# Kernel optimization log

Measured on AMD Instinct MI355X. Metric: run time of the kernel, lower is better.

## Reference

```python
import jax, jax.numpy as jnp
import numpy as np

# ---- config (mirrors argparse-config of dnc_model) ----
T, B, IN = 64, 32, 64          # time-major input [T,B,IN]
N, Wd, R, NW = 512, 64, 4, 1   # memory_size, word_size, num_reads, num_writes
H, OUT = 256, 64               # controller hidden, output_size
CLIP = 20.0
EPS = 1e-6
IF = R*Wd + R + NW*Wd + NW + NW*Wd + NW*Wd + R + NW + NW + R*(1+2*NW)  # interface size = 471
CTRL_IN = IN + R*Wd


def setup_inputs() -> dict:
    key = jax.random.key(0)
    ks = jax.random.split(key, 6)
    g = lambda k, shape, s: (jax.random.normal(k, shape, jnp.float32) * s)
    return {
        "inputs": g(ks[0], (T, B, IN), 1.0),
        "Wx": g(ks[1], (CTRL_IN, 4*H), 0.05),
        "Wh": g(ks[2], (H, 4*H), 0.05),
        "b_lstm": jnp.zeros((4*H,), jnp.float32),
        "W_if": g(ks[3], (H, IF), 0.05),
        "b_if": jnp.zeros((IF,), jnp.float32),
        "W_out": g(ks[4], (H + R*Wd, OUT), 0.05),
        "b_out": jnp.zeros((OUT,), jnp.float32),
    }


def _clip(x):
    return jnp.clip(x, -CLIP, CLIP)


def _oneplus(x):
    return 1.0 + jax.nn.softplus(x)


def _content_weights(memory, keys, strengths):
    # memory [B,N,Wd], keys [B,K,Wd], strengths [B,K] -> softmax cosine weights [B,K,N]
    dot = jnp.einsum('bkw,bnw->bkn', keys, memory)
    mn = jnp.sqrt(jnp.sum(memory * memory, -1))          # [B,N]
    kn = jnp.sqrt(jnp.sum(keys * keys, -1))              # [B,K]
    sim = dot / (kn[..., None] * mn[:, None, :] + EPS)
    return jax.nn.softmax(sim * strengths[..., None], axis=-1)


def _allocation(usage):
    # usage [B,N] -> allocation weights [B,N] (sorted-free-list scheme)
    u = EPS + (1.0 - EPS) * usage
    idx = jnp.argsort(u, axis=-1)                        # ascending usage
    su = jnp.take_along_axis(u, idx, -1)
    cp = jnp.cumprod(su, axis=-1)
    excl = jnp.concatenate([jnp.ones_like(cp[:, :1]), cp[:, :-1]], -1)
    a_sorted = (1.0 - su) * excl
    inv = jnp.argsort(idx, axis=-1)
    return jnp.take_along_axis(a_sorted, inv, -1)


def _dnc_forward(inputs, Wx, Wh, b_lstm, W_if, b_if, W_out, b_out):
    eye = jnp.eye(N, dtype=inputs.dtype)

    def step(carry, x_t):
        h, c, mem, rw, ww_prev, link, prec, usage, reads = carry
        # ---- controller LSTM (prev read vectors fed in) ----
        ctrl_in = jnp.concatenate([x_t, reads.reshape(B, R*Wd)], -1)
        gates = ctrl_in @ Wx + h @ Wh + b_lstm
        ig, fg, gg, og = jnp.split(gates, 4, -1)
        c = jax.nn.sigmoid(fg) * c + jax.nn.sigmoid(ig) * jnp.tanh(gg)
        h = jax.nn.sigmoid(og) * jnp.tanh(c)
        hc, cc = _clip(h), _clip(c)
        # ---- interface vector ----
        itf = hc @ W_if + b_if
        off = 0
        read_keys = itf[:, off:off+R*Wd].reshape(B, R, Wd); off += R*Wd
        read_str = _oneplus(itf[:, off:off+R]); off += R
        write_keys = itf[:, off:off+NW*Wd].reshape(B, NW, Wd); off += NW*Wd
        write_str = _oneplus(itf[:, off:off+NW]); off += NW
        erase = jax.nn.sigmoid(itf[:, off:off+NW*Wd]).reshape(B, NW, Wd); off += NW*Wd
        write_vecs = itf[:, off:off+NW*Wd].reshape(B, NW, Wd); off += NW*Wd
        free_g = jax.nn.sigmoid(itf[:, off:off+R]); off += R
        alloc_g = jax.nn.sigmoid(itf[:, off:off+NW]); off += NW
        write_g = jax.nn.sigmoid(itf[:, off:off+NW]); off += NW
        modes = jax.nn.softmax(itf[:, off:off+R*(1+2*NW)].reshape(B, R, 1+2*NW), -1)
        bwd_mode = modes[..., :NW]
        fwd_mode = modes[..., NW:2*NW]
        content_mode = modes[..., 2*NW]
        # ---- usage update (uses prev write/read weights) ----
        u = usage + (1.0 - usage) * (1.0 - jnp.prod(1.0 - ww_prev, axis=1))
        psi = jnp.prod(1.0 - free_g[..., None] * rw, axis=1)
        usage = u * psi
        # ---- write weights: allocation + content ----
        allocs = []
        u_run = usage
        for hd in range(NW):
            a = _allocation(u_run)
            allocs.append(a)
            u_run = u_run + (1.0 - u_run) * (write_g[:, hd:hd+1] * alloc_g[:, hd:hd+1]) * a
        alloc = jnp.stack(allocs, 1)                      # [B,NW,N]
        wc = _content_weights(mem, write_keys, write_str) # [B,NW,N]
        ww = write_g[..., None] * (alloc_g[..., None] * alloc + (1.0 - alloc_g[..., None]) * wc)
        # ---- erase / add write ----
        erase_w = ww[..., None] * erase[:, :, None, :]    # [B,NW,N,Wd]
        mem = mem * jnp.prod(1.0 - erase_w, axis=1) + jnp.einsum('bhn,bhw->bnw', ww, write_vecs)
        # ---- temporal link + precedence ----
        w_i = ww[..., :, None]
        w_j = ww[..., None, :]
        link = (1.0 - w_i - w_j) * link + w_i * prec[..., None, :]
        link = link * (1.0 - eye)
        prec = (1.0 - ww.sum(-1, keepdims=True)) * prec + ww
        # ---- read weights: content + forward/backward linkage ----
        rc = _content_weights(mem, read_keys, read_str)   # [B,R,N]
        fw = jnp.einsum('bhij,brj->brhi', link, rw)       # forward  [B,R,NW,N]
        bw = jnp.einsum('bhji,brj->brhi', link, rw)       # backward [B,R,NW,N]
        rw = (content_mode[..., None] * rc
              + jnp.einsum('brh,brhn->brn', fwd_mode, fw)
              + jnp.einsum('brh,brhn->brn', bwd_mode, bw))
        reads = jnp.einsum('brn,bnw->brw', rw, mem)       # [B,R,Wd]
        out = _clip(jnp.concatenate([hc, reads.reshape(B, R*Wd)], -1) @ W_out + b_out)
        return (hc, cc, mem, rw, ww, link, prec, usage, reads), out

    z = jnp.zeros
    dt = inputs.dtype
    carry0 = (z((B, H), dt), z((B, H), dt), z((B, N, Wd), dt), z((B, R, N), dt),
              z((B, NW, N), dt), z((B, NW, N, N), dt), z((B, NW, N), dt),
              z((B, N), dt), z((B, R, Wd), dt))
    _, outs = jax.lax.scan(step, carry0, inputs)
    return outs  # [T, B, OUT]


def reference(inputs, Wx, Wh, b_lstm, W_if, b_if, W_out, b_out):
    return _dnc_forward(inputs, Wx, Wh, b_lstm, W_if, b_if, W_out, b_out)
```

## Files before the change

kernel.cpp:

```cpp
#include <hip/hip_runtime.h>
#include <math.h>

#define Tn 64
#define Bn 32
#define INn 64
#define Nn 512
#define WDn 64
#define Rn 4
#define Hn 256
#define G4H 1024
#define OUTn 64
#define IFn 471
#define CLIPV 20.0f
#define EPSV 1e-6f

#define OFF_RKEY 0
#define OFF_RSTR 256
#define OFF_WKEY 260
#define OFF_WSTR 324
#define OFF_ERASE 325
#define OFF_WVEC 389
#define OFF_FREE 453
#define OFF_AG 457
#define OFF_WG 458
#define OFF_MODES 459

__device__ float S_h[2][Bn][Hn];
__device__ float S_c[2][Bn][Hn];
__device__ float S_gates[2][Bn][G4H];
__device__ float S_mem[Bn][Nn][WDn];
__device__ float S_rw[Bn][Rn][Nn];
__device__ float S_ww[2][Bn][Nn];
__device__ float S_link[Bn][Nn][Nn];
__device__ float S_prec[2][Bn][Nn];
__device__ float S_usage[2][Bn][Nn];
__device__ float S_reads[Bn][Rn][WDn];
__device__ float S_itf[Bn][IFn];
__device__ float S_rc[Bn][Rn][Nn];
__device__ float S_fw[Bn][Rn][Nn];
__device__ float S_bwp[Bn][8][Rn*Nn];
__device__ float S_sumww[Bn];
__device__ unsigned int g_ww[Bn];
__device__ unsigned int g_rc[Bn];
__device__ unsigned int g_ld[Bn];
__device__ unsigned int g_fin;

__device__ __forceinline__ float sigm(float x){ return 1.f/(1.f+expf(-x)); }
__device__ __forceinline__ float clipv(float x){ return fminf(fmaxf(x,-CLIPV),CLIPV); }
__device__ __forceinline__ float oneplusf(float x){
  float sp = (x > 0.f) ? (x + log1pf(expf(-x))) : log1pf(expf(x));
  return 1.f + sp;
}
__device__ __forceinline__ float wredsum(float v){
  #pragma unroll
  for (int o=32;o>0;o>>=1) v += __shfl_xor(v,o,64);
  return v;
}
__device__ __forceinline__ float bredsum(float v, volatile float* scr){
  v = wredsum(v);
  if ((threadIdx.x & 63) == 0) scr[threadIdx.x >> 6] = v;
  __syncthreads();
  float s = scr[0];
  #pragma unroll
  for (int i=1;i<8;i++) s += scr[i];
  __syncthreads();
  return s;
}
__device__ __forceinline__ float bredmax(float v, volatile float* scr){
  #pragma unroll
  for (int o=32;o>0;o>>=1) v = fmaxf(v,__shfl_xor(v,o,64));
  if ((threadIdx.x & 63) == 0) scr[threadIdx.x >> 6] = v;
  __syncthreads();
  float m = scr[0];
  #pragma unroll
  for (int i=1;i<8;i++) m = fmaxf(m, scr[i]);
  __syncthreads();
  return m;
}
__device__ __forceinline__ void sig_release(unsigned int* flag){
  __builtin_amdgcn_fence(__ATOMIC_RELEASE, "agent");
  __hip_atomic_fetch_add(flag, 1u, __ATOMIC_RELAXED, __HIP_MEMORY_SCOPE_AGENT);
}
__device__ __forceinline__ void spin_until(unsigned int* flag, unsigned int target){
  while (__hip_atomic_load(flag, __ATOMIC_RELAXED, __HIP_MEMORY_SCOPE_AGENT) < target)
    __builtin_amdgcn_s_sleep(8);
}

extern "C" __global__ void __launch_bounds__(256)
k_init(){
  size_t g = (size_t)blockIdx.x*256 + threadIdx.x;
  size_t stride = (size_t)gridDim.x*256;
  float* lk = &S_link[0][0][0];
  for (size_t i=g; i<(size_t)Bn*Nn*Nn; i+=stride) lk[i]=0.f;
  float* mm = &S_mem[0][0][0];
  for (size_t i=g; i<(size_t)Bn*Nn*WDn; i+=stride) mm[i]=0.f;
  float* rr = &S_rw[0][0][0];
  for (size_t i=g; i<(size_t)Bn*Rn*Nn; i+=stride) rr[i]=0.f;
  float* rd = &S_reads[0][0][0];
  for (size_t i=g; i<(size_t)Bn*Rn*WDn; i+=stride) rd[i]=0.f;
  for (size_t i=g; i<(size_t)2*Bn*Nn; i+=stride){
    S_ww[0][0][i]=0.f; S_prec[0][0][i]=0.f; S_usage[0][0][i]=0.f;
  }
  for (size_t i=g; i<(size_t)2*Bn*Hn; i+=stride){
    S_h[0][0][i]=0.f; S_c[0][0][i]=0.f;
  }
  if (blockIdx.x==0){
    if (threadIdx.x < Bn){ g_ww[threadIdx.x]=0u; g_rc[threadIdx.x]=0u; g_ld[threadIdx.x]=0u; }
    if (threadIdx.x == 0) g_fin=0u;
  }
}

struct ShG { float ctrl[Bn][65]; };

__device__ __forceinline__ void gates_core(ShG& sg, int tn, int jt,
        const float* __restrict__ xin, const float* __restrict__ Wx,
        const float* __restrict__ Wh, const float* __restrict__ b_lstm){
  const int tid = threadIdx.x, lane = tid & 63, wvi = tid >> 6;
  const int j = jt*64 + lane;
  const int hp = (tn+1)&1;
  const int b0 = wvi*4;
  float bias = b_lstm[j];
  float a0=bias, a1=bias, a2=bias, a3=bias;
  for (int c=0;c<9;++c){
    #pragma unroll
    for (int u=0;u<4;u++){
      int e = u*512 + tid;
      int b2 = e >> 6, kk = e & 63;
      float v;
      if (c==0)       v = xin[((size_t)tn*Bn + b2)*INn + kk];
      else if (c<5)   v = ((const float*)S_reads[b2])[(c-1)*64 + kk];
      else            v = S_h[hp][b2][(c-5)*64 + kk];
      sg.ctrl[b2][kk] = v;
    }
    __syncthreads();
    const float* wb = (c<5) ? (Wx + (size_t)(c*64)*G4H + j)
                            : (Wh + (size_t)((c-5)*64)*G4H + j);
    #pragma unroll
    for (int kk=0;kk<64;kk++){
      float wv = wb[(size_t)kk*G4H];
      a0 += sg.ctrl[b0+0][kk]*wv;
      a1 += sg.ctrl[b0+1][kk]*wv;
      a2 += sg.ctrl[b0+2][kk]*wv;
      a3 += sg.ctrl[b0+3][kk]*wv;
    }
    __syncthreads();
  }
  const int gs = tn&1;
  S_gates[gs][b0+0][j]=a0;
  S_gates[gs][b0+1][j]=a1;
  S_gates[gs][b0+2][j]=a2;
  S_gates[gs][b0+3][j]=a3;
}

extern "C" __global__ void __launch_bounds__(512)
k_gates_pro(const float* __restrict__ xin, const float* __restrict__ Wx,
            const float* __restrict__ Wh, const float* __restrict__ b_lstm){
  __shared__ ShG sg;
  gates_core(sg, 0, blockIdx.x, xin, Wx, Wh, b_lstm);
}

struct ShA {
  float hc[Hn];
  float itf[IFn];
  unsigned long long keys[Nn];
  float alloc[Nn];
  float sim[Nn];
  float rsim[Rn][Nn];
  float tile[64][65];
  float wkey[WDn];
  float rk[Rn][WDn];
  float er[WDn];
  float wv[WDn];
  float red[8];
  float knw, knr[Rn], betar[Rn];
};
struct ShL {
  float ww[Nn];
  float prec[Nn];
  float rw[Rn][Nn];
  float bwp4[4][Rn][Nn];
};
struct ShF {
  float fw[Rn][Nn];
  float bw[Rn][Nn];
  float rc[Rn][Nn];
  float modes[Rn][4];
  float part[8][Rn][WDn];
  float vin[512];
};
union ShU { ShA a; ShL l; ShF f; ShG g; };

extern "C" __global__ void __launch_bounds__(512, 4)
k_step(int t, const float* __restrict__ xin,
       const float* __restrict__ Wx, const float* __restrict__ Wh,
       const float* __restrict__ b_lstm,
       const float* __restrict__ W_if, const float* __restrict__ b_if,
       const float* __restrict__ W_out, const float* __restrict__ b_out,
       float* __restrict__ outp){
  __shared__ ShU sh;
  const int tid = threadIdx.x;
  const int lane = tid & 63, wvi = tid >> 6;
  const int bid = blockIdx.x;
  const int cur = t&1, prev = cur^1;

  if (bid < 32){
    const int b = bid;
    if (tid < Hn){
      int h = tid;
      float g0=S_gates[cur][b][h],     g1=S_gates[cur][b][Hn+h];
      float g2=S_gates[cur][b][2*Hn+h],g3=S_gates[cur][b][3*Hn+h];
      float cold = S_c[prev][b][h];
      float cn = sigm(g1)*cold + sigm(g0)*tanhf(g2);
      float hn = sigm(g3)*tanhf(cn);
      float hcv = clipv(hn);
      S_c[cur][b][h] = clipv(cn);
      S_h[cur][b][h] = hcv;
      sh.a.hc[h] = hcv;
    }
    __syncthreads();
    if (tid < IFn){
      float acc = b_if[tid];
      for (int k=0;k<Hn;k+=8){
        float s = 0.f;
        #pragma unroll
        for (int u=0;u<8;u++) s += sh.a.hc[k+u]*W_if[(size_t)(k+u)*IFn + tid];
        acc += s;
      }
      sh.a.itf[tid] = acc;
      S_itf[b][tid] = acc;
    }
    __syncthreads();
    if (tid < WDn){
      sh.a.wkey[tid] = sh.a.itf[OFF_WKEY+tid];
      sh.a.er[tid]   = sigm(sh.a.itf[OFF_ERASE+tid]);
      sh.a.wv[tid]   = sh.a.itf[OFF_WVEC+tid];
    } else if (tid < WDn + Rn*WDn){
      int k2 = tid - WDn;
      sh.a.rk[k2>>6][k2&63] = sh.a.itf[OFF_RKEY + k2];
    }
    {
      float fg0=sigm(sh.a.itf[OFF_FREE+0]), fg1=sigm(sh.a.itf[OFF_FREE+1]);
      float fg2=sigm(sh.a.itf[OFF_FREE+2]), fg3=sigm(sh.a.itf[OFF_FREE+3]);
      int n = tid;
      float uu = S_usage[prev][b][n], wwp = S_ww[prev][b][n];
      float u = uu + (1.f-uu)*wwp;
      float psi = (1.f - fg0*S_rw[b][0][n])*(1.f - fg1*S_rw[b][1][n])
                * (1.f - fg2*S_rw[b][2][n])*(1.f - fg3*S_rw[b][3][n]);
      float un = u*psi;
      S_usage[cur][b][n] = un;
      float v = EPSV + (1.f-EPSV)*un;
      sh.a.keys[n] = ((unsigned long long)__float_as_uint(v) << 32) | (unsigned)n;
    }
    __syncthreads();
    if (wvi==0){
      float kv = sh.a.wkey[lane];
      float s2 = wredsum(kv*kv);
      if (lane==0) sh.a.knw = sqrtf(s2);
    } else if (wvi<=4){
      int r = wvi-1;
      float kv = sh.a.rk[r][lane];
      float s2 = wredsum(kv*kv);
      if (lane==0) sh.a.knr[r] = sqrtf(s2);
    } else if (wvi==5 && lane<4){
      sh.a.betar[lane] = oneplusf(sh.a.itf[OFF_RSTR+lane]);
    }
    {
      unsigned long long myk = sh.a.keys[tid];
      float prod = 1.f;
      for (int j=0;j<Nn;j+=8){
        #pragma unroll
        for (int u=0;u<8;u++){
          unsigned long long kj = sh.a.keys[j+u];
          float uj = __uint_as_float((unsigned)(kj>>32));
          prod *= (kj < myk) ? uj : 1.f;
        }
      }
      float myu = __uint_as_float((unsigned)(myk>>32));
      sh.a.alloc[tid] = (1.f - myu)*prod;
    }
    __syncthreads();
    float betaw = oneplusf(sh.a.itf[OFF_WSTR]);
    for (int tile=0;tile<8;tile++){
      #pragma unroll
      for (int u=0;u<8;u++){
        int e = u*512 + tid;
        int nn = e>>6, w = e&63;
        sh.a.tile[nn][w] = S_mem[b][tile*64+nn][w];
      }
      __syncthreads();
      {
        int nn = tid>>3, qq = tid&7;
        float d=0.f, nrm=0.f;
        #pragma unroll
        for (int i=0;i<8;i++){
          int w = qq*8+i;
          float m = sh.a.tile[nn][w];
          d += m*sh.a.wkey[w]; nrm += m*m;
        }
        #pragma unroll
        for (int o=1;o<8;o<<=1){ d += __shfl_xor(d,o,64); nrm += __shfl_xor(nrm,o,64); }
        if (qq==0){
          int n = tile*64+nn;
          sh.a.sim[n] = betaw * d / (sh.a.knw*sqrtf(nrm) + EPSV);
        }
      }
      __syncthreads();
    }
    {
      float v = sh.a.sim[tid];
      float mx = bredmax(v, sh.a.red);
      float e = expf(v - mx);
      float ssum = bredsum(e, sh.a.red);
      float wc = e/ssum;
      float ag = sigm(sh.a.itf[OFF_AG]);
      float wg = sigm(sh.a.itf[OFF_WG]);
      float wwv = wg*(ag*sh.a.alloc[tid] + (1.f-ag)*wc);
      S_ww[cur][b][tid] = wwv;
      float wsum = bredsum(wwv, sh.a.red);
      if (tid==0) S_sumww[b] = wsum;
      sh.a.alloc[tid] = wwv;
    }
    __syncthreads();
    if (tid==0) sig_release(&g_ww[b]);
    for (int tile=0;tile<8;tile++){
      #pragma unroll
      for (int u=0;u<8;u++){
        int e = u*512 + tid;
        int nn = e>>6, w = e&63;
        int n = tile*64+nn;
        float m = S_mem[b][n][w];
        float wwn = sh.a.alloc[n];
        m = m*(1.f - wwn*sh.a.er[w]) + wwn*sh.a.wv[w];
        S_mem[b][n][w] = m;
        sh.a.tile[nn][w] = m;
      }
      __syncthreads();
      {
        int nn = tid>>3, qq = tid&7;
        float a0=0.f,a1=0.f,a2=0.f,a3=0.f,nrm=0.f;
        #pragma unroll
        for (int i=0;i<8;i++){
          int w = qq*8+i;
          float m = sh.a.tile[nn][w];
          a0 += m*sh.a.rk[0][w]; a1 += m*sh.a.rk[1][w];
          a2 += m*sh.a.rk[2][w]; a3 += m*sh.a.rk[3][w];
          nrm += m*m;
        }
        #pragma unroll
        for (int o=1;o<8;o<<=1){
          a0 += __shfl_xor(a0,o,64); a1 += __shfl_xor(a1,o,64);
          a2 += __shfl_xor(a2,o,64); a3 += __shfl_xor(a3,o,64);
          nrm += __shfl_xor(nrm,o,64);
        }
        if (qq==0){
          int n = tile*64+nn;
          float mn = sqrtf(nrm);
          sh.a.rsim[0][n] = sh.a.betar[0]*a0/(sh.a.knr[0]*mn + EPSV);
          sh.a.rsim[1][n] = sh.a.betar[1]*a1/(sh.a.knr[1]*mn + EPSV);
          sh.a.rsim[2][n] = sh.a.betar[2]*a2/(sh.a.knr[2]*mn + EPSV);
          sh.a.rsim[3][n] = sh.a.betar[3]*a3/(sh.a.knr[3]*mn + EPSV);
        }
      }
      __syncthreads();
    }
    for (int r=0;r<Rn;r++){
      float v = sh.a.rsim[r][tid];
      float mx = bredmax(v, sh.a.red);
      float e = expf(v - mx);
      float ssum = bredsum(e, sh.a.red);
      S_rc[b][r][tid] = e/ssum;
    }
    __syncthreads();
    if (tid==0) sig_release(&g_rc[b]);

  } else if (bid < 288){
    const int idx = bid - 32;
    const int b = idx >> 3, ch = idx & 7;
    const int i0 = ch*64;
    if (tid==0){
      spin_until(&g_ww[b], (unsigned)(t+1));
      __builtin_amdgcn_fence(__ATOMIC_ACQUIRE, "agent");
    }
    __syncthreads();
    sh.l.ww[tid]   = S_ww[cur][b][tid];
    sh.l.prec[tid] = S_prec[prev][b][tid];
    for (int k=tid;k<Rn*Nn;k+=512) ((float*)sh.l.rw)[k] = ((const float*)S_rw[b])[k];
    __syncthreads();
    float sumww = S_sumww[b];
    float wj[2][4], pj[2][4], rj[4][2][4];
    #pragma unroll
    for (int jjc=0;jjc<2;jjc++){
      float4 w4 = ((const float4*)sh.l.ww)[jjc*64+lane];
      float4 p4 = ((const float4*)sh.l.prec)[jjc*64+lane];
      wj[jjc][0]=w4.x; wj[jjc][1]=w4.y; wj[jjc][2]=w4.z; wj[jjc][3]=w4.w;
      pj[jjc][0]=p4.x; pj[jjc][1]=p4.y; pj[jjc][2]=p4.z; pj[jjc][3]=p4.w;
      #pragma unroll
      for (int r=0;r<4;r++){
        float4 r4 = ((const float4*)sh.l.rw[r])[jjc*64+lane];
        rj[r][jjc][0]=r4.x; rj[r][jjc][1]=r4.y; rj[r][jjc][2]=r4.z; rj[r][jjc][3]=r4.w;
      }
    }
    float bwa[4][2][4];
    #pragma unroll
    for (int r=0;r<4;r++)
      #pragma unroll
      for (int jjc=0;jjc<2;jjc++)
        #pragma unroll
        for (int s=0;s<4;s++) bwa[r][jjc][s]=0.f;
    for (int rr=0;rr<8;rr++){
      const int i = i0 + wvi*8 + rr;
      float wi = sh.l.ww[i];
      float ci = 1.f - wi;
      float ri[4] = {sh.l.rw[0][i], sh.l.rw[1][i], sh.l.rw[2][i], sh.l.rw[3][i]};
      float f[4] = {0.f,0.f,0.f,0.f};
      float4* lrow4 = (float4*)(&S_link[b][i][0]);
      #pragma unroll
      for (int jjc=0;jjc<2;jjc++){
        float4 L4 = lrow4[jjc*64+lane];
        float Ls[4] = {L4.x, L4.y, L4.z, L4.w};
        #pragma unroll
        for (int s=0;s<4;s++){
          float Ln = (ci - wj[jjc][s])*Ls[s] + wi*pj[jjc][s];
          int j = jjc*256 + lane*4 + s;
          Ln = (j==i) ? 0.f : Ln;
          Ls[s] = Ln;
          #pragma unroll
          for (int r=0;r<4;r++){
            f[r] += Ln*rj[r][jjc][s];
            bwa[r][jjc][s] += Ln*ri[r];
          }
        }
        float4 Lo; Lo.x=Ls[0]; Lo.y=Ls[1]; Lo.z=Ls[2]; Lo.w=Ls[3];
        lrow4[jjc*64+lane] = Lo;
      }
      #pragma unroll
      for (int r=0;r<4;r++){
        float fr = wredsum(f[r]);
        if (lane==0) S_fw[b][r][i] = fr;
      }
    }
    if (wvi < 4){
      #pragma unroll
      for (int r=0;r<4;r++)
        #pragma unroll
        for (int jjc=0;jjc<2;jjc++){
          float4 v4; v4.x=bwa[r][jjc][0]; v4.y=bwa[r][jjc][1]; v4.z=bwa[r][jjc][2]; v4.w=bwa[r][jjc][3];
          ((float4*)sh.l.bwp4[wvi][r])[jjc*64+lane] = v4;
        }
    }
    __syncthreads();
    if (wvi >= 4){
      int v = wvi-4;
      #pragma unroll
      for (int r=0;r<4;r++)
        #pragma unroll
        for (int jjc=0;jjc<2;jjc++){
          float4 v4 = ((float4*)sh.l.bwp4[v][r])[jjc*64+lane];
          v4.x+=bwa[r][jjc][0]; v4.y+=bwa[r][jjc][1]; v4.z+=bwa[r][jjc][2]; v4.w+=bwa[r][jjc][3];
          ((float4*)sh.l.bwp4[v][r])[jjc*64+lane] = v4;
        }
    }
    __syncthreads();
    for (int k=tid;k<Rn*Nn;k+=512){
      float s = ((float*)sh.l.bwp4[0])[k] + ((float*)sh.l.bwp4[1])[k]
              + ((float*)sh.l.bwp4[2])[k] + ((float*)sh.l.bwp4[3])[k];
      S_bwp[b][ch][k] = s;
    }
    if (tid < 64){
      int j = i0 + tid;
      S_prec[cur][b][j] = (1.f - sumww)*sh.l.prec[j] + sh.l.ww[j];
    }
    __syncthreads();
    if (tid==0) sig_release(&g_ld[b]);

  } else if (bid < 320){
    const int b = bid - 288;
    if (tid==0){
      spin_until(&g_ld[b], 8u*(unsigned)(t+1));
      spin_until(&g_rc[b], (unsigned)(t+1));
      __builtin_amdgcn_fence(__ATOMIC_ACQUIRE, "agent");
    }
    __syncthreads();
    for (int k=tid;k<Rn*Nn;k+=512){
      ((float*)sh.f.fw)[k] = ((const float*)S_fw[b])[k];
      float sbw = 0.f;
      #pragma unroll
      for (int ch=0;ch<8;ch++) sbw += S_bwp[b][ch][k];
      ((float*)sh.f.bw)[k] = sbw;
      ((float*)sh.f.rc)[k] = ((const float*)S_rc[b])[k];
    }
    if (tid < 4){
      int r = tid;
      float m0 = S_itf[b][OFF_MODES + r*3 + 0];
      float m1 = S_itf[b][OFF_MODES + r*3 + 1];
      float m2 = S_itf[b][OFF_MODES + r*3 + 2];
      float mx = fmaxf(m0,fmaxf(m1,m2));
      float e0=expf(m0-mx), e1=expf(m1-mx), e2=expf(m2-mx);
      float si = e0+e1+e2;
      sh.f.modes[r][0]=e0/si; sh.f.modes[r][1]=e1/si; sh.f.modes[r][2]=e2/si;
    }
    __syncthreads();
    for (int k=tid;k<Rn*Nn;k+=512){
      int r = k>>9, n = k&511;
      float v = sh.f.modes[r][2]*sh.f.rc[r][n] + sh.f.modes[r][1]*sh.f.fw[r][n]
              + sh.f.modes[r][0]*sh.f.bw[r][n];
      sh.f.rc[r][n] = v;
      S_rw[b][r][n] = v;
    }
    __syncthreads();
    {
      float a0=0.f,a1=0.f,a2=0.f,a3=0.f;
      #pragma unroll 4
      for (int nn=0;nn<64;nn++){
        int n = wvi*64+nn;
        float m = S_mem[b][n][lane];
        a0 += sh.f.rc[0][n]*m; a1 += sh.f.rc[1][n]*m;
        a2 += sh.f.rc[2][n]*m; a3 += sh.f.rc[3][n]*m;
      }
      sh.f.part[wvi][0][lane]=a0; sh.f.part[wvi][1][lane]=a1;
      sh.f.part[wvi][2][lane]=a2; sh.f.part[wvi][3][lane]=a3;
    }
    __syncthreads();
    if (tid < 256){
      int r = tid>>6, w = tid&63;
      float sv = 0.f;
      #pragma unroll
      for (int v=0;v<8;v++) sv += sh.f.part[v][r][w];
      S_reads[b][r][w] = sv;
      sh.f.vin[256+tid] = sv;
      sh.f.vin[tid] = S_h[cur][b][tid];
    }
    __syncthreads();
    {
      int qq = tid>>6, o = tid&63;
      float sacc = 0.f;
      for (int k2=qq*64;k2<qq*64+64;k2+=8){
        #pragma unroll
        for (int u=0;u<8;u++) sacc += sh.f.vin[k2+u]*W_out[(size_t)(k2+u)*OUTn + o];
      }
      sh.f.part[qq][0][o] = sacc;
    }
    __syncthreads();
    if (tid < 64){
      float sv = b_out[tid];
      #pragma unroll
      for (int qq=0;qq<8;qq++) sv += sh.f.part[qq][0][tid];
      outp[((size_t)t*Bn + b)*OUTn + tid] = clipv(sv);
    }
    __syncthreads();
    if (tid==0) sig_release(&g_fin);

  } else {
    if (t+1 >= Tn) return;
    const int jt = bid - 320;
    if (tid==0){
      spin_until(&g_fin, 32u*(unsigned)(t+1));
      __builtin_amdgcn_fence(__ATOMIC_ACQUIRE, "agent");
    }
    __syncthreads();
    gates_core(sh.g, t+1, jt, xin, Wx, Wh, b_lstm);
  }
}

extern "C" void kernel_launch(void* const* d_in, const int* in_sizes, int n_in,
                              void* d_out, int out_size, void* d_ws, size_t ws_size,
                              hipStream_t stream){
  (void)in_sizes; (void)n_in; (void)d_ws; (void)ws_size; (void)out_size;
  const float* xin = (const float*)d_in[0];
  const float* Wx  = (const float*)d_in[1];
  const float* Wh  = (const float*)d_in[2];
  const float* bl  = (const float*)d_in[3];
  const float* Wif = (const float*)d_in[4];
  const float* bif = (const float*)d_in[5];
  const float* Wo  = (const float*)d_in[6];
  const float* bo  = (const float*)d_in[7];
  hipLaunchKernelGGL(k_init, dim3(1024), dim3(256), 0, stream);
  hipLaunchKernelGGL(k_gates_pro, dim3(16), dim3(512), 0, stream, xin, Wx, Wh, bl);
  for (int t=0; t<Tn; ++t){
    hipLaunchKernelGGL(k_step, dim3(336), dim3(512), 0, stream,
                       t, xin, Wx, Wh, bl, Wif, bif, Wo, bo, (float*)d_out);
  }
}
```

Measured before the change: 7.154 ms.

## Fuse per-timestep launches into one persistent kernel with flag-based dependencies

```diff
diff --git a/kernel.cpp b/kernel.cpp
--- a/kernel.cpp
+++ b/kernel.cpp
@@ -40,10 +40,13 @@
 __device__ float S_fw[Bn][Rn][Nn];
 __device__ float S_bwp[Bn][8][Rn*Nn];
 __device__ float S_sumww[Bn];
+__device__ unsigned int g_hh;
 __device__ unsigned int g_ww[Bn];
 __device__ unsigned int g_rc[Bn];
 __device__ unsigned int g_ld[Bn];
+__device__ unsigned int g_fb[Bn];
 __device__ unsigned int g_fin;
+__device__ unsigned int g_gate;
 
 __device__ __forceinline__ float sigm(float x){ return 1.f/(1.f+expf(-x)); }
 __device__ __forceinline__ float clipv(float x){ return fminf(fmaxf(x,-CLIPV),CLIPV); }
@@ -83,7 +86,23 @@
 }
 __device__ __forceinline__ void spin_until(unsigned int* flag, unsigned int target){
   while (__hip_atomic_load(flag, __ATOMIC_RELAXED, __HIP_MEMORY_SCOPE_AGENT) < target)
-    __builtin_amdgcn_s_sleep(8);
+    __builtin_amdgcn_s_sleep(2);
+}
+__device__ __forceinline__ void wait_acq1(unsigned int* f, unsigned int tgt){
+  if (threadIdx.x==0){
+    spin_until(f, tgt);
+    __builtin_amdgcn_fence(__ATOMIC_ACQUIRE, "agent");
+  }
+  __syncthreads();
+}
+__device__ __forceinline__ void wait_acq2(unsigned int* f1, unsigned int t1,
+                                          unsigned int* f2, unsigned int t2){
+  if (threadIdx.x==0){
+    spin_until(f1, t1);
+    spin_until(f2, t2);
+    __builtin_amdgcn_fence(__ATOMIC_ACQUIRE, "agent");
+  }
+  __syncthreads();
 }
 
 extern "C" __global__ void __launch_bounds__(256)
@@ -105,60 +124,14 @@
     S_h[0][0][i]=0.f; S_c[0][0][i]=0.f;
   }
   if (blockIdx.x==0){
-    if (threadIdx.x < Bn){ g_ww[threadIdx.x]=0u; g_rc[threadIdx.x]=0u; g_ld[threadIdx.x]=0u; }
-    if (threadIdx.x == 0) g_fin=0u;
+    if (threadIdx.x < Bn){
+      g_ww[threadIdx.x]=0u; g_rc[threadIdx.x]=0u; g_ld[threadIdx.x]=0u; g_fb[threadIdx.x]=0u;
+    }
+    if (threadIdx.x == 0){ g_fin=0u; g_gate=0u; g_hh=0u; }
   }
 }
 
 struct ShG { float ctrl[Bn][65]; };
-
-__device__ __forceinline__ void gates_core(ShG& sg, int tn, int jt,
-        const float* __restrict__ xin, const float* __restrict__ Wx,
-        const float* __restrict__ Wh, const float* __restrict__ b_lstm){
-  const int tid = threadIdx.x, lane = tid & 63, wvi = tid >> 6;
-  const int j = jt*64 + lane;
-  const int hp = (tn+1)&1;
-  const int b0 = wvi*4;
-  float bias = b_lstm[j];
-  float a0=bias, a1=bias, a2=bias, a3=bias;
-  for (int c=0;c<9;++c){
-    #pragma unroll
-    for (int u=0;u<4;u++){
-      int e = u*512 + tid;
-      int b2 = e >> 6, kk = e & 63;
-      float v;
-      if (c==0)       v = xin[((size_t)tn*Bn + b2)*INn + kk];
-      else if (c<5)   v = ((const float*)S_reads[b2])[(c-1)*64 + kk];
-      else            v = S_h[hp][b2][(c-5)*64 + kk];
-      sg.ctrl[b2][kk] = v;
-    }
-    __syncthreads();
-    const float* wb = (c<5) ? (Wx + (size_t)(c*64)*G4H + j)
-                            : (Wh + (size_t)((c-5)*64)*G4H + j);
-    #pragma unroll
-    for (int kk=0;kk<64;kk++){
-      float wv = wb[(size_t)kk*G4H];
-      a0 += sg.ctrl[b0+0][kk]*wv;
-      a1 += sg.ctrl[b0+1][kk]*wv;
-      a2 += sg.ctrl[b0+2][kk]*wv;
-      a3 += sg.ctrl[b0+3][kk]*wv;
-    }
-    __syncthreads();
-  }
-  const int gs = tn&1;
-  S_gates[gs][b0+0][j]=a0;
-  S_gates[gs][b0+1][j]=a1;
-  S_gates[gs][b0+2][j]=a2;
-  S_gates[gs][b0+3][j]=a3;
-}
-
-extern "C" __global__ void __launch_bounds__(512)
-k_gates_pro(const float* __restrict__ xin, const float* __restrict__ Wx,
-            const float* __restrict__ Wh, const float* __restrict__ b_lstm){
-  __shared__ ShG sg;
-  gates_core(sg, 0, blockIdx.x, xin, Wx, Wh, b_lstm);
-}
-
 struct ShA {
   float hc[Hn];
   float itf[IFn];
@@ -191,374 +164,430 @@
 union ShU { ShA a; ShL l; ShF f; ShG g; };
 
 extern "C" __global__ void __launch_bounds__(512, 4)
-k_step(int t, const float* __restrict__ xin,
-       const float* __restrict__ Wx, const float* __restrict__ Wh,
-       const float* __restrict__ b_lstm,
-       const float* __restrict__ W_if, const float* __restrict__ b_if,
-       const float* __restrict__ W_out, const float* __restrict__ b_out,
-       float* __restrict__ outp){
+k_all(const float* __restrict__ xin,
+      const float* __restrict__ Wx, const float* __restrict__ Wh,
+      const float* __restrict__ b_lstm,
+      const float* __restrict__ W_if, const float* __restrict__ b_if,
+      const float* __restrict__ W_out, const float* __restrict__ b_out,
+      float* __restrict__ outp){
   __shared__ ShU sh;
   const int tid = threadIdx.x;
   const int lane = tid & 63, wvi = tid >> 6;
   const int bid = blockIdx.x;
-  const int cur = t&1, prev = cur^1;
 
   if (bid < 32){
     const int b = bid;
-    if (tid < Hn){
-      int h = tid;
-      float g0=S_gates[cur][b][h],     g1=S_gates[cur][b][Hn+h];
-      float g2=S_gates[cur][b][2*Hn+h],g3=S_gates[cur][b][3*Hn+h];
-      float cold = S_c[prev][b][h];
-      float cn = sigm(g1)*cold + sigm(g0)*tanhf(g2);
-      float hn = sigm(g3)*tanhf(cn);
-      float hcv = clipv(hn);
-      S_c[cur][b][h] = clipv(cn);
-      S_h[cur][b][h] = hcv;
-      sh.a.hc[h] = hcv;
+    for (int t=0; t<Tn; ++t){
+      const int cur = t&1, prev = cur^1;
+      wait_acq2(&g_gate, 16u*(unsigned)(t+1), &g_fb[b], (unsigned)t);
+      if (tid < Hn){
+        int h = tid;
+        float g0=S_gates[cur][b][h],     g1=S_gates[cur][b][Hn+h];
+        float g2=S_gates[cur][b][2*Hn+h],g3=S_gates[cur][b][3*Hn+h];
+        float cold = S_c[prev][b][h];
+        float cn = sigm(g1)*cold + sigm(g0)*tanhf(g2);
+        float hn = sigm(g3)*tanhf(cn);
+        float hcv = clipv(hn);
+        S_c[cur][b][h] = clipv(cn);
+        S_h[cur][b][h] = hcv;
+        sh.a.hc[h] = hcv;
+      }
+      __syncthreads();
+      if (tid==0) sig_release(&g_hh);
+      if (tid < IFn){
+        float acc = b_if[tid];
+        for (int k=0;k<Hn;k+=8){
+          float s = 0.f;
+          #pragma unroll
+          for (int u=0;u<8;u++) s += sh.a.hc[k+u]*W_if[(size_t)(k+u)*IFn + tid];
+          acc += s;
+        }
+        sh.a.itf[tid] = acc;
+        S_itf[b][tid] = acc;
+      }
+      __syncthreads();
+      if (tid < WDn){
+        sh.a.wkey[tid] = sh.a.itf[OFF_WKEY+tid];
+        sh.a.er[tid]   = sigm(sh.a.itf[OFF_ERASE+tid]);
+        sh.a.wv[tid]   = sh.a.itf[OFF_WVEC+tid];
+      } else if (tid < WDn + Rn*WDn){
+        int k2 = tid - WDn;
+        sh.a.rk[k2>>6][k2&63] = sh.a.itf[OFF_RKEY + k2];
+      }
+      {
+        float fg0=sigm(sh.a.itf[OFF_FREE+0]), fg1=sigm(sh.a.itf[OFF_FREE+1]);
+        float fg2=sigm(sh.a.itf[OFF_FREE+2]), fg3=sigm(sh.a.itf[OFF_FREE+3]);
+        int n = tid;
+        float uu = S_usage[prev][b][n], wwp = S_ww[prev][b][n];
+        float u = uu + (1.f-uu)*wwp;
+        float psi = (1.f - fg0*S_rw[b][0][n])*(1.f - fg1*S_rw[b][1][n])
+                  * (1.f - fg2*S_rw[b][2][n])*(1.f - fg3*S_rw[b][3][n]);
+        float un = u*psi;
+        S_usage[cur][b][n] = un;
+        float v = EPSV + (1.f-EPSV)*un;
+        sh.a.keys[n] = ((unsigned long long)__float_as_uint(v) << 32) | (unsigned)n;
+      }
+      __syncthreads();
+      if (wvi==0){
+        float kv = sh.a.wkey[lane];
+        float s2 = wredsum(kv*kv);
+        if (lane==0) sh.a.knw = sqrtf(s2);
+      } else if (wvi<=4){
+        int r = wvi-1;
+        float kv = sh.a.rk[r][lane];
+        float s2 = wredsum(kv*kv);
+        if (lane==0) sh.a.knr[r] = sqrtf(s2);
+      } else if (wvi==5 && lane<4){
+        sh.a.betar[lane] = oneplusf(sh.a.itf[OFF_RSTR+lane]);
+      }
+      {
+        unsigned long long myk = sh.a.keys[tid];
+        float prod = 1.f;
+        for (int j=0;j<Nn;j+=8){
+          #pragma unroll
+          for (int u=0;u<8;u++){
+            unsigned long long kj = sh.a.keys[j+u];
+            float uj = __uint_as_float((unsigned)(kj>>32));
+            prod *= (kj < myk) ? uj : 1.f;
+          }
+        }
+        float myu = __uint_as_float((unsigned)(myk>>32));
+        sh.a.alloc[tid] = (1.f - myu)*prod;
+      }
+      __syncthreads();
+      float betaw = oneplusf(sh.a.itf[OFF_WSTR]);
+      for (int tile=0;tile<8;tile++){
+        #pragma unroll
+        for (int u=0;u<8;u++){
+          int e = u*512 + tid;
+          int nn = e>>6, w = e&63;
+          sh.a.tile[nn][w] = S_mem[b][tile*64+nn][w];
+        }
+        __syncthreads();
+        {
+          int nn = tid>>3, qq = tid&7;
+          float d=0.f, nrm=0.f;
+          #pragma unroll
+          for (int i=0;i<8;i++){
+            int w = qq*8+i;
+            float m = sh.a.tile[nn][w];
+            d += m*sh.a.wkey[w]; nrm += m*m;
+          }
+          #pragma unroll
+          for (int o=1;o<8;o<<=1){ d += __shfl_xor(d,o,64); nrm += __shfl_xor(nrm,o,64); }
+          if (qq==0){
+            int n = tile*64+nn;
+            sh.a.sim[n] = betaw * d / (sh.a.knw*sqrtf(nrm) + EPSV);
+          }
+        }
+        __syncthreads();
+      }
+      {
+        float v = sh.a.sim[tid];
+        float mx = bredmax(v, sh.a.red);
+        float e = expf(v - mx);
+        float ssum = bredsum(e, sh.a.red);
+        float wc = e/ssum;
+        float ag = sigm(sh.a.itf[OFF_AG]);
+        float wg = sigm(sh.a.itf[OFF_WG]);
+        float wwv = wg*(ag*sh.a.alloc[tid] + (1.f-ag)*wc);
+        S_ww[cur][b][tid] = wwv;
+        float wsum = bredsum(wwv, sh.a.red);
+        if (tid==0) S_sumww[b] = wsum;
+        sh.a.alloc[tid] = wwv;
+      }
+      __syncthreads();
+      if (tid==0) sig_release(&g_ww[b]);
+      for (int tile=0;tile<8;tile++){
+        #pragma unroll
+        for (int u=0;u<8;u++){
+          int e = u*512 + tid;
+          int nn = e>>6, w = e&63;
+          int n = tile*64+nn;
+          float m = S_mem[b][n][w];
+          float wwn = sh.a.alloc[n];
+          m = m*(1.f - wwn*sh.a.er[w]) + wwn*sh.a.wv[w];
+          S_mem[b][n][w] = m;
+          sh.a.tile[nn][w] = m;
+        }
+        __syncthreads();
+        {
+          int nn = tid>>3, qq = tid&7;
+          float a0=0.f,a1=0.f,a2=0.f,a3=0.f,nrm=0.f;
+          #pragma unroll
+          for (int i=0;i<8;i++){
+            int w = qq*8+i;
+            float m = sh.a.tile[nn][w];
+            a0 += m*sh.a.rk[0][w]; a1 += m*sh.a.rk[1][w];
+            a2 += m*sh.a.rk[2][w]; a3 += m*sh.a.rk[3][w];
+            nrm += m*m;
+          }
+          #pragma unroll
+          for (int o=1;o<8;o<<=1){
+            a0 += __shfl_xor(a0,o,64); a1 += __shfl_xor(a1,o,64);
+            a2 += __shfl_xor(a2,o,64); a3 += __shfl_xor(a3,o,64);
+            nrm += __shfl_xor(nrm,o,64);
+          }
+          if (qq==0){
+            int n = tile*64+nn;
+            float mn = sqrtf(nrm);
+            sh.a.rsim[0][n] = sh.a.betar[0]*a0/(sh.a.knr[0]*mn + EPSV);
+            sh.a.rsim[1][n] = sh.a.betar[1]*a1/(sh.a.knr[1]*mn + EPSV);
+            sh.a.rsim[2][n] = sh.a.betar[2]*a2/(sh.a.knr[2]*mn + EPSV);
+            sh.a.rsim[3][n] = sh.a.betar[3]*a3/(sh.a.knr[3]*mn + EPSV);
+          }
+        }
+        __syncthreads();
+      }
+      for (int r=0;r<Rn;r++){
+        float v = sh.a.rsim[r][tid];
+        float mx = bredmax(v, sh.a.red);
+        float e = expf(v - mx);
+        float ssum = bredsum(e, sh.a.red);
+        S_rc[b][r][tid] = e/ssum;
+      }
+      __syncthreads();
+      if (tid==0) sig_release(&g_rc[b]);
     }
-    __syncthreads();
-    if (tid < IFn){
-      float acc = b_if[tid];
-      for (int k=0;k<Hn;k+=8){
-        float s = 0.f;
-        #pragma unroll
-        for (int u=0;u<8;u++) s += sh.a.hc[k+u]*W_if[(size_t)(k+u)*IFn + tid];
-        acc += s;
-      }
-      sh.a.itf[tid] = acc;
-      S_itf[b][tid] = acc;
-    }
-    __syncthreads();
-    if (tid < WDn){
-      sh.a.wkey[tid] = sh.a.itf[OFF_WKEY+tid];
-      sh.a.er[tid]   = sigm(sh.a.itf[OFF_ERASE+tid]);
-      sh.a.wv[tid]   = sh.a.itf[OFF_WVEC+tid];
-    } else if (tid < WDn + Rn*WDn){
-      int k2 = tid - WDn;
-      sh.a.rk[k2>>6][k2&63] = sh.a.itf[OFF_RKEY + k2];
-    }
-    {
-      float fg0=sigm(sh.a.itf[OFF_FREE+0]), fg1=sigm(sh.a.itf[OFF_FREE+1]);
-      float fg2=sigm(sh.a.itf[OFF_FREE+2]), fg3=sigm(sh.a.itf[OFF_FREE+3]);
-      int n = tid;
-      float uu = S_usage[prev][b][n], wwp = S_ww[prev][b][n];
-      float u = uu + (1.f-uu)*wwp;
-      float psi = (1.f - fg0*S_rw[b][0][n])*(1.f - fg1*S_rw[b][1][n])
-                * (1.f - fg2*S_rw[b][2][n])*(1.f - fg3*S_rw[b][3][n]);
-      float un = u*psi;
-      S_usage[cur][b][n] = un;
-      float v = EPSV + (1.f-EPSV)*un;
-      sh.a.keys[n] = ((unsigned long long)__float_as_uint(v) << 32) | (unsigned)n;
-    }
-    __syncthreads();
-    if (wvi==0){
-      float kv = sh.a.wkey[lane];
-      float s2 = wredsum(kv*kv);
-      if (lane==0) sh.a.knw = sqrtf(s2);
-    } else if (wvi<=4){
-      int r = wvi-1;
-      float kv = sh.a.rk[r][lane];
-      float s2 = wredsum(kv*kv);
-      if (lane==0) sh.a.knr[r] = sqrtf(s2);
-    } else if (wvi==5 && lane<4){
-      sh.a.betar[lane] = oneplusf(sh.a.itf[OFF_RSTR+lane]);
-    }
-    {
-      unsigned long long myk = sh.a.keys[tid];
-      float prod = 1.f;
-      for (int j=0;j<Nn;j+=8){
-        #pragma unroll
-        for (int u=0;u<8;u++){
-          unsigned long long kj = sh.a.keys[j+u];
-          float uj = __uint_as_float((unsigned)(kj>>32));
-          prod *= (kj < myk) ? uj : 1.f;
-        }
-      }
-      float myu = __uint_as_float((unsigned)(myk>>32));
-      sh.a.alloc[tid] = (1.f - myu)*prod;
-    }
-    __syncthreads();
-    float betaw = oneplusf(sh.a.itf[OFF_WSTR]);
-    for (int tile=0;tile<8;tile++){
-      #pragma unroll
-      for (int u=0;u<8;u++){
-        int e = u*512 + tid;
-        int nn = e>>6, w = e&63;
-        sh.a.tile[nn][w] = S_mem[b][tile*64+nn][w];
-      }
-      __syncthreads();
-      {
-        int nn = tid>>3, qq = tid&7;
-        float d=0.f, nrm=0.f;
-        #pragma unroll
-        for (int i=0;i<8;i++){
-          int w = qq*8+i;
-          float m = sh.a.tile[nn][w];
-          d += m*sh.a.wkey[w]; nrm += m*m;
-        }
-        #pragma unroll
-        for (int o=1;o<8;o<<=1){ d += __shfl_xor(d,o,64); nrm += __shfl_xor(nrm,o,64); }
-        if (qq==0){
-          int n = tile*64+nn;
-          sh.a.sim[n] = betaw * d / (sh.a.knw*sqrtf(nrm) + EPSV);
-        }
-      }
-      __syncthreads();
-    }
-    {
-      float v = sh.a.sim[tid];
-      float mx = bredmax(v, sh.a.red);
-      float e = expf(v - mx);
-      float ssum = bredsum(e, sh.a.red);
-      float wc = e/ssum;
-      float ag = sigm(sh.a.itf[OFF_AG]);
-      float wg = sigm(sh.a.itf[OFF_WG]);
-      float wwv = wg*(ag*sh.a.alloc[tid] + (1.f-ag)*wc);
-      S_ww[cur][b][tid] = wwv;
-      float wsum = bredsum(wwv, sh.a.red);
-      if (tid==0) S_sumww[b] = wsum;
-      sh.a.alloc[tid] = wwv;
-    }
-    __syncthreads();
-    if (tid==0) sig_release(&g_ww[b]);
-    for (int tile=0;tile<8;tile++){
-      #pragma unroll
-      for (int u=0;u<8;u++){
-        int e = u*512 + tid;
-        int nn = e>>6, w = e&63;
-        int n = tile*64+nn;
-        float m = S_mem[b][n][w];
-        float wwn = sh.a.alloc[n];
-        m = m*(1.f - wwn*sh.a.er[w]) + wwn*sh.a.wv[w];
-        S_mem[b][n][w] = m;
-        sh.a.tile[nn][w] = m;
-      }
-      __syncthreads();
-      {
-        int nn = tid>>3, qq = tid&7;
-        float a0=0.f,a1=0.f,a2=0.f,a3=0.f,nrm=0.f;
-        #pragma unroll
-        for (int i=0;i<8;i++){
-          int w = qq*8+i;
-          float m = sh.a.tile[nn][w];
-          a0 += m*sh.a.rk[0][w]; a1 += m*sh.a.rk[1][w];
-          a2 += m*sh.a.rk[2][w]; a3 += m*sh.a.rk[3][w];
-          nrm += m*m;
-        }
-        #pragma unroll
-        for (int o=1;o<8;o<<=1){
-          a0 += __shfl_xor(a0,o,64); a1 += __shfl_xor(a1,o,64);
-          a2 += __shfl_xor(a2,o,64); a3 += __shfl_xor(a3,o,64);
-          nrm += __shfl_xor(nrm,o,64);
-        }
-        if (qq==0){
-          int n = tile*64+nn;
-          float mn = sqrtf(nrm);
-          sh.a.rsim[0][n] = sh.a.betar[0]*a0/(sh.a.knr[0]*mn + EPSV);
-          sh.a.rsim[1][n] = sh.a.betar[1]*a1/(sh.a.knr[1]*mn + EPSV);
-          sh.a.rsim[2][n] = sh.a.betar[2]*a2/(sh.a.knr[2]*mn + EPSV);
-          sh.a.rsim[3][n] = sh.a.betar[3]*a3/(sh.a.knr[3]*mn + EPSV);
-        }
-      }
-      __syncthreads();
-    }
-    for (int r=0;r<Rn;r++){
-      float v = sh.a.rsim[r][tid];
-      float mx = bredmax(v, sh.a.red);
-      float e = expf(v - mx);
-      float ssum = bredsum(e, sh.a.red);
-      S_rc[b][r][tid] = e/ssum;
-    }
-    __syncthreads();
-    if (tid==0) sig_release(&g_rc[b]);
 
   } else if (bid < 288){
     const int idx = bid - 32;
     const int b = idx >> 3, ch = idx & 7;
     const int i0 = ch*64;
-    if (tid==0){
-      spin_until(&g_ww[b], (unsigned)(t+1));
-      __builtin_amdgcn_fence(__ATOMIC_ACQUIRE, "agent");
-    }
-    __syncthreads();
-    sh.l.ww[tid]   = S_ww[cur][b][tid];
-    sh.l.prec[tid] = S_prec[prev][b][tid];
-    for (int k=tid;k<Rn*Nn;k+=512) ((float*)sh.l.rw)[k] = ((const float*)S_rw[b])[k];
-    __syncthreads();
-    float sumww = S_sumww[b];
-    float wj[2][4], pj[2][4], rj[4][2][4];
-    #pragma unroll
-    for (int jjc=0;jjc<2;jjc++){
-      float4 w4 = ((const float4*)sh.l.ww)[jjc*64+lane];
-      float4 p4 = ((const float4*)sh.l.prec)[jjc*64+lane];
-      wj[jjc][0]=w4.x; wj[jjc][1]=w4.y; wj[jjc][2]=w4.z; wj[jjc][3]=w4.w;
-      pj[jjc][0]=p4.x; pj[jjc][1]=p4.y; pj[jjc][2]=p4.z; pj[jjc][3]=p4.w;
-      #pragma unroll
-      for (int r=0;r<4;r++){
-        float4 r4 = ((const float4*)sh.l.rw[r])[jjc*64+lane];
-        rj[r][jjc][0]=r4.x; rj[r][jjc][1]=r4.y; rj[r][jjc][2]=r4.z; rj[r][jjc][3]=r4.w;
-      }
-    }
-    float bwa[4][2][4];
-    #pragma unroll
-    for (int r=0;r<4;r++)
-      #pragma unroll
-      for (int jjc=0;jjc<2;jjc++)
-        #pragma unroll
-        for (int s=0;s<4;s++) bwa[r][jjc][s]=0.f;
-    for (int rr=0;rr<8;rr++){
-      const int i = i0 + wvi*8 + rr;
-      float wi = sh.l.ww[i];
-      float ci = 1.f - wi;
-      float ri[4] = {sh.l.rw[0][i], sh.l.rw[1][i], sh.l.rw[2][i], sh.l.rw[3][i]};
-      float f[4] = {0.f,0.f,0.f,0.f};
-      float4* lrow4 = (float4*)(&S_link[b][i][0]);
+    for (int t=0; t<Tn; ++t){
+      const int cur = t&1, prev = cur^1;
+      wait_acq1(&g_ww[b], (unsigned)(t+1));
+      sh.l.ww[tid]   = S_ww[cur][b][tid];
+      sh.l.prec[tid] = S_prec[prev][b][tid];
+      for (int k=tid;k<Rn*Nn;k+=512) ((float*)sh.l.rw)[k] = ((const float*)S_rw[b])[k];
+      __syncthreads();
+      float sumww = S_sumww[b];
+      float wj[2][4], pj[2][4], rj[4][2][4];
       #pragma unroll
       for (int jjc=0;jjc<2;jjc++){
-        float4 L4 = lrow4[jjc*64+lane];
-        float Ls[4] = {L4.x, L4.y, L4.z, L4.w};
-        #pragma unroll
-        for (int s=0;s<4;s++){
-          float Ln = (ci - wj[jjc][s])*Ls[s] + wi*pj[jjc][s];
-          int j = jjc*256 + lane*4 + s;
-          Ln = (j==i) ? 0.f : Ln;
-          Ls[s] = Ln;
-          #pragma unroll
-          for (int r=0;r<4;r++){
-            f[r] += Ln*rj[r][jjc][s];
-            bwa[r][jjc][s] += Ln*ri[r];
-          }
-        }
-        float4 Lo; Lo.x=Ls[0]; Lo.y=Ls[1]; Lo.z=Ls[2]; Lo.w=Ls[3];
-        lrow4[jjc*64+lane] = Lo;
-      }
-      #pragma unroll
-      for (int r=0;r<4;r++){
-        float fr = wredsum(f[r]);
-        if (lane==0) S_fw[b][r][i] = fr;
-      }
-    }
-    if (wvi < 4){
+        float4 w4 = ((const float4*)sh.l.ww)[jjc*64+lane];
+        float4 p4 = ((const float4*)sh.l.prec)[jjc*64+lane];
+        wj[jjc][0]=w4.x; wj[jjc][1]=w4.y; wj[jjc][2]=w4.z; wj[jjc][3]=w4.w;
+        pj[jjc][0]=p4.x; pj[jjc][1]=p4.y; pj[jjc][2]=p4.z; pj[jjc][3]=p4.w;
+        #pragma unroll
+        for (int r=0;r<4;r++){
+          float4 r4 = ((const float4*)sh.l.rw[r])[jjc*64+lane];
+          rj[r][jjc][0]=r4.x; rj[r][jjc][1]=r4.y; rj[r][jjc][2]=r4.z; rj[r][jjc][3]=r4.w;
+        }
+      }
+      float bwa[4][2][4];
       #pragma unroll
       for (int r=0;r<4;r++)
         #pragma unroll
+        for (int jjc=0;jjc<2;jjc++)
+          #pragma unroll
+          for (int s=0;s<4;s++) bwa[r][jjc][s]=0.f;
+      for (int rr=0;rr<8;rr++){
+        const int i = i0 + wvi*8 + rr;
+        float wi = sh.l.ww[i];
+        float ci = 1.f - wi;
+        float ri[4] = {sh.l.rw[0][i], sh.l.rw[1][i], sh.l.rw[2][i], sh.l.rw[3][i]};
+        float f[4] = {0.f,0.f,0.f,0.f};
+        float4* lrow4 = (float4*)(&S_link[b][i][0]);
+        #pragma unroll
         for (int jjc=0;jjc<2;jjc++){
-          float4 v4; v4.x=bwa[r][jjc][0]; v4.y=bwa[r][jjc][1]; v4.z=bwa[r][jjc][2]; v4.w=bwa[r][jjc][3];
-          ((float4*)sh.l.bwp4[wvi][r])[jjc*64+lane] = v4;
-        }
+          float4 L4 = lrow4[jjc*64+lane];
+          float Ls[4] = {L4.x, L4.y, L4.z, L4.w};
+          #pragma unroll
+          for (int s=0;s<4;s++){
+            float Ln = (ci - wj[jjc][s])*Ls[s] + wi*pj[jjc][s];
+            int j = jjc*256 + lane*4 + s;
+            Ln = (j==i) ? 0.f : Ln;
+            Ls[s] = Ln;
+            #pragma unroll
+            for (int r=0;r<4;r++){
+              f[r] += Ln*rj[r][jjc][s];
+              bwa[r][jjc][s] += Ln*ri[r];
+            }
+          }
+          float4 Lo; Lo.x=Ls[0]; Lo.y=Ls[1]; Lo.z=Ls[2]; Lo.w=Ls[3];
+          lrow4[jjc*64+lane] = Lo;
+        }
+        #pragma unroll
+        for (int r=0;r<4;r++){
+          float fr = wredsum(f[r]);
+          if (lane==0) S_fw[b][r][i] = fr;
+        }
+      }
+      if (wvi < 4){
+        #pragma unroll
+        for (int r=0;r<4;r++)
+          #pragma unroll
+          for (int jjc=0;jjc<2;jjc++){
+            float4 v4; v4.x=bwa[r][jjc][0]; v4.y=bwa[r][jjc][1]; v4.z=bwa[r][jjc][2]; v4.w=bwa[r][jjc][3];
+            ((float4*)sh.l.bwp4[wvi][r])[jjc*64+lane] = v4;
+          }
+      }
+      __syncthreads();
+      if (wvi >= 4){
+        int v = wvi-4;
+        #pragma unroll
+        for (int r=0;r<4;r++)
+          #pragma unroll
+          for (int jjc=0;jjc<2;jjc++){
+            float4 v4 = ((float4*)sh.l.bwp4[v][r])[jjc*64+lane];
+            v4.x+=bwa[r][jjc][0]; v4.y+=bwa[r][jjc][1]; v4.z+=bwa[r][jjc][2]; v4.w+=bwa[r][jjc][3];
+            ((float4*)sh.l.bwp4[v][r])[jjc*64+lane] = v4;
+          }
+      }
+      __syncthreads();
+      for (int k=tid;k<Rn*Nn;k+=512){
+        float s = ((float*)sh.l.bwp4[0])[k] + ((float*)sh.l.bwp4[1])[k]
+                + ((float*)sh.l.bwp4[2])[k] + ((float*)sh.l.bwp4[3])[k];
+        S_bwp[b][ch][k] = s;
+      }
+      if (tid < 64){
+        int j = i0 + tid;
+        S_prec[cur][b][j] = (1.f - sumww)*sh.l.prec[j] + sh.l.ww[j];
+      }
+      __syncthreads();
+      if (tid==0) sig_release(&g_ld[b]);
     }
-    __syncthreads();
-    if (wvi >= 4){
-      int v = wvi-4;
-      #pragma unroll
-      for (int r=0;r<4;r++)
-        #pragma unroll
-        for (int jjc=0;jjc<2;jjc++){
-          float4 v4 = ((float4*)sh.l.bwp4[v][r])[jjc*64+lane];
-          v4.x+=bwa[r][jjc][0]; v4.y+=bwa[r][jjc][1]; v4.z+=bwa[r][jjc][2]; v4.w+=bwa[r][jjc][3];
-          ((float4*)sh.l.bwp4[v][r])[jjc*64+lane] = v4;
-        }
-    }
-    __syncthreads();
-    for (int k=tid;k<Rn*Nn;k+=512){
-      float s = ((float*)sh.l.bwp4[0])[k] + ((float*)sh.l.bwp4[1])[k]
-              + ((float*)sh.l.bwp4[2])[k] + ((float*)sh.l.bwp4[3])[k];
-      S_bwp[b][ch][k] = s;
-    }
-    if (tid < 64){
-      int j = i0 + tid;
-      S_prec[cur][b][j] = (1.f - sumww)*sh.l.prec[j] + sh.l.ww[j];
-    }
-    __syncthreads();
-    if (tid==0) sig_release(&g_ld[b]);
 
   } else if (bid < 320){
     const int b = bid - 288;
-    if (tid==0){
-      spin_until(&g_ld[b], 8u*(unsigned)(t+1));
-      spin_until(&g_rc[b], (unsigned)(t+1));
-      __builtin_amdgcn_fence(__ATOMIC_ACQUIRE, "agent");
+    for (int t=0; t<Tn; ++t){
+      const int cur = t&1;
+      wait_acq2(&g_ld[b], 8u*(unsigned)(t+1), &g_rc[b], (unsigned)(t+1));
+      for (int k=tid;k<Rn*Nn;k+=512){
+        ((float*)sh.f.fw)[k] = ((const float*)S_fw[b])[k];
+        float sbw = 0.f;
+        #pragma unroll
+        for (int ch=0;ch<8;ch++) sbw += S_bwp[b][ch][k];
+        ((float*)sh.f.bw)[k] = sbw;
+        ((float*)sh.f.rc)[k] = ((const float*)S_rc[b])[k];
+      }
+      if (tid < 4){
+        int r = tid;
+        float m0 = S_itf[b][OFF_MODES + r*3 + 0];
+        float m1 = S_itf[b][OFF_MODES + r*3 + 1];
+        float m2 = S_itf[b][OFF_MODES + r*3 + 2];
+        float mx = fmaxf(m0,fmaxf(m1,m2));
+        float e0=expf(m0-mx), e1=expf(m1-mx), e2=expf(m2-mx);
+        float si = e0+e1+e2;
+        sh.f.modes[r][0]=e0/si; sh.f.modes[r][1]=e1/si; sh.f.modes[r][2]=e2/si;
+      }
+      __syncthreads();
+      for (int k=tid;k<Rn*Nn;k+=512){
+        int r = k>>9, n = k&511;
+        float v = sh.f.modes[r][2]*sh.f.rc[r][n] + sh.f.modes[r][1]*sh.f.fw[r][n]
+                + sh.f.modes[r][0]*sh.f.bw[r][n];
+        sh.f.rc[r][n] = v;
+        S_rw[b][r][n] = v;
+      }
+      __syncthreads();
+      {
+        float a0=0.f,a1=0.f,a2=0.f,a3=0.f;
+        #pragma unroll 4
+        for (int nn=0;nn<64;nn++){
+          int n = wvi*64+nn;
+          float m = S_mem[b][n][lane];
+          a0 += sh.f.rc[0][n]*m; a1 += sh.f.rc[1][n]*m;
+          a2 += sh.f.rc[2][n]*m; a3 += sh.f.rc[3][n]*m;
+        }
+        sh.f.part[wvi][0][lane]=a0; sh.f.part[wvi][1][lane]=a1;
+        sh.f.part[wvi][2][lane]=a2; sh.f.part[wvi][3][lane]=a3;
+      }
+      __syncthreads();
+      if (tid < 256){
+        int r = tid>>6, w = tid&63;
+        float sv = 0.f;
+        #pragma unroll
+        for (int v=0;v<8;v++) sv += sh.f.part[v][r][w];
+        S_reads[b][r][w] = sv;
+        sh.f.vin[256+tid] = sv;
+        sh.f.vin[tid] = S_h[cur][b][tid];
+      }
+      __syncthreads();
+      {
+        int qq = tid>>6, o = tid&63;
+        float sacc = 0.f;
+        for (int k2=qq*64;k2<qq*64+64;k2+=8){
+          #pragma unroll
+          for (int u=0;u<8;u++) sacc += sh.f.vin[k2+u]*W_out[(size_t)(k2+u)*OUTn + o];
+        }
+        sh.f.part[qq][0][o] = sacc;
+      }
+      __syncthreads();
+      if (tid < 64){
+        float sv = b_out[tid];
+        #pragma unroll
+        for (int qq=0;qq<8;qq++) sv += sh.f.part[qq][0][tid];
+        outp[((size_t)t*Bn + b)*OUTn + tid] = clipv(sv);
+      }
+      __syncthreads();
+      if (tid==0){
+        __builtin_amdgcn_fence(__ATOMIC_RELEASE, "agent");
+        __hip_atomic_fetch_add(&g_fb[b], 1u, __ATOMIC_RELAXED, __HIP_MEMORY_SCOPE_AGENT);
+        __hip_atomic_fetch_add(&g_fin, 1u, __ATOMIC_RELAXED, __HIP_MEMORY_SCOPE_AGENT);
+      }
     }
-    __syncthreads();
-    for (int k=tid;k<Rn*Nn;k+=512){
-      ((float*)sh.f.fw)[k] = ((const float*)S_fw[b])[k];
-      float sbw = 0.f;
-      #pragma unroll
-      for (int ch=0;ch<8;ch++) sbw += S_bwp[b][ch][k];
-      ((float*)sh.f.bw)[k] = sbw;
-      ((float*)sh.f.rc)[k] = ((const float*)S_rc[b])[k];
+
+  } else {
+    const int jt = bid - 320;
+    const int j = jt*64 + lane;
+    const int b0 = wvi*4;
+    for (int t=0; t<Tn; ++t){
+      const int hp = (t+1)&1;
+      float bias = b_lstm[j];
+      float a0=bias, a1=bias, a2=bias, a3=bias;
+      wait_acq1(&g_hh, 32u*(unsigned)t);
+      for (int c=0;c<5;++c){
+        #pragma unroll
+        for (int u=0;u<4;u++){
+          int e = u*512 + tid;
+          int b2 = e >> 6, kk = e & 63;
+          float v;
+          if (c==0) v = xin[((size_t)t*Bn + b2)*INn + kk];
+          else      v = S_h[hp][b2][(c-1)*64 + kk];
+          sh.g.ctrl[b2][kk] = v;
+        }
+        __syncthreads();
+        const float* wb = (c==0) ? (Wx + (size_t)0*G4H + j)
+                                 : (Wh + (size_t)((c-1)*64)*G4H + j);
+        #pragma unroll
+        for (int kk=0;kk<64;kk++){
+          float wv = wb[(size_t)kk*G4H];
+          a0 += sh.g.ctrl[b0+0][kk]*wv;
+          a1 += sh.g.ctrl[b0+1][kk]*wv;
+          a2 += sh.g.ctrl[b0+2][kk]*wv;
+          a3 += sh.g.ctrl[b0+3][kk]*wv;
+        }
+        __syncthreads();
+      }
+      wait_acq1(&g_fin, 32u*(unsigned)t);
+      for (int c=0;c<4;++c){
+        #pragma unroll
+        for (int u=0;u<4;u++){
+          int e = u*512 + tid;
+          int b2 = e >> 6, kk = e & 63;
+          sh.g.ctrl[b2][kk] = ((const float*)S_reads[b2])[c*64 + kk];
+        }
+        __syncthreads();
+        const float* wb = Wx + (size_t)(INn + c*64)*G4H + j;
+        #pragma unroll
+        for (int kk=0;kk<64;kk++){
+          float wv = wb[(size_t)kk*G4H];
+          a0 += sh.g.ctrl[b0+0][kk]*wv;
+          a1 += sh.g.ctrl[b0+1][kk]*wv;
+          a2 += sh.g.ctrl[b0+2][kk]*wv;
+          a3 += sh.g.ctrl[b0+3][kk]*wv;
+        }
+        __syncthreads();
+      }
+      const int gs = t&1;
+      S_gates[gs][b0+0][j]=a0;
+      S_gates[gs][b0+1][j]=a1;
+      S_gates[gs][b0+2][j]=a2;
+      S_gates[gs][b0+3][j]=a3;
+      __syncthreads();
+      if (tid==0) sig_release(&g_gate);
     }
-    if (tid < 4){
-      int r = tid;
-      float m0 = S_itf[b][OFF_MODES + r*3 + 0];
-      float m1 = S_itf[b][OFF_MODES + r*3 + 1];
-      float m2 = S_itf[b][OFF_MODES + r*3 + 2];
-      float mx = fmaxf(m0,fmaxf(m1,m2));
-      float e0=expf(m0-mx), e1=expf(m1-mx), e2=expf(m2-mx);
-      float si = e0+e1+e2;
-      sh.f.modes[r][0]=e0/si; sh.f.modes[r][1]=e1/si; sh.f.modes[r][2]=e2/si;
-    }
-    __syncthreads();
-    for (int k=tid;k<Rn*Nn;k+=512){
-      int r = k>>9, n = k&511;
-      float v = sh.f.modes[r][2]*sh.f.rc[r][n] + sh.f.modes[r][1]*sh.f.fw[r][n]
-              + sh.f.modes[r][0]*sh.f.bw[r][n];
-      sh.f.rc[r][n] = v;
-      S_rw[b][r][n] = v;
-    }
-    __syncthreads();
-    {
-      float a0=0.f,a1=0.f,a2=0.f,a3=0.f;
-      #pragma unroll 4
-      for (int nn=0;nn<64;nn++){
-        int n = wvi*64+nn;
-        float m = S_mem[b][n][lane];
-        a0 += sh.f.rc[0][n]*m; a1 += sh.f.rc[1][n]*m;
-        a2 += sh.f.rc[2][n]*m; a3 += sh.f.rc[3][n]*m;
-      }
-      sh.f.part[wvi][0][lane]=a0; sh.f.part[wvi][1][lane]=a1;
-      sh.f.part[wvi][2][lane]=a2; sh.f.part[wvi][3][lane]=a3;
-    }
-    __syncthreads();
-    if (tid < 256){
-      int r = tid>>6, w = tid&63;
-      float sv = 0.f;
-      #pragma unroll
-      for (int v=0;v<8;v++) sv += sh.f.part[v][r][w];
-      S_reads[b][r][w] = sv;
-      sh.f.vin[256+tid] = sv;
-      sh.f.vin[tid] = S_h[cur][b][tid];
-    }
-    __syncthreads();
-    {
-      int qq = tid>>6, o = tid&63;
-      float sacc = 0.f;
-      for (int k2=qq*64;k2<qq*64+64;k2+=8){
-        #pragma unroll
-        for (int u=0;u<8;u++) sacc += sh.f.vin[k2+u]*W_out[(size_t)(k2+u)*OUTn + o];
-      }
-      sh.f.part[qq][0][o] = sacc;
-    }
-    __syncthreads();
-    if (tid < 64){
-      float sv = b_out[tid];
-      #pragma unroll
-      for (int qq=0;qq<8;qq++) sv += sh.f.part[qq][0][tid];
-      outp[((size_t)t*Bn + b)*OUTn + tid] = clipv(sv);
-    }
-    __syncthreads();
-    if (tid==0) sig_release(&g_fin);
-
-  } else {
-    if (t+1 >= Tn) return;
-    const int jt = bid - 320;
-    if (tid==0){
-      spin_until(&g_fin, 32u*(unsigned)(t+1));
-      __builtin_amdgcn_fence(__ATOMIC_ACQUIRE, "agent");
-    }
-    __syncthreads();
-    gates_core(sh.g, t+1, jt, xin, Wx, Wh, b_lstm);
   }
 }
 
@@ -575,9 +604,6 @@
   const float* Wo  = (const float*)d_in[6];
   const float* bo  = (const float*)d_in[7];
   hipLaunchKernelGGL(k_init, dim3(1024), dim3(256), 0, stream);
-  hipLaunchKernelGGL(k_gates_pro, dim3(16), dim3(512), 0, stream, xin, Wx, Wh, bl);
-  for (int t=0; t<Tn; ++t){
-    hipLaunchKernelGGL(k_step, dim3(336), dim3(512), 0, stream,
-                       t, xin, Wx, Wh, bl, Wif, bif, Wo, bo, (float*)d_out);
-  }
-}
+  hipLaunchKernelGGL(k_all, dim3(336), dim3(512), 0, stream,
+                     xin, Wx, Wh, bl, Wif, bif, Wo, bo, (float*)d_out);
+}
```

Result: slower. 15.00 ms (+109.6%).
